# Performance work log

Hardware: AMD Instinct MI355X
Metric: run time of the kernel (lower is better)

Reference implementation:

```python
import jax, jax.numpy as jnp
import numpy as np

N_HEAD, DIM, D_K, D_V = 16, 1024, 64, 64
B, L = 4, 2048


def setup_inputs() -> dict:
    key = jax.random.key(0)
    ks = jax.random.split(key, 8)
    def xavier(k, shape, fan_in, fan_out):
        std = float(np.sqrt(2.0 / (fan_in + fan_out)))
        return jax.random.normal(k, shape, dtype=jnp.float32) * std
    return {
        "q": jax.random.normal(ks[0], (B, L, DIM), dtype=jnp.float32),
        "k": jax.random.normal(ks[1], (B, L, DIM), dtype=jnp.float32),
        "v": jax.random.normal(ks[2], (B, L, DIM), dtype=jnp.float32),
        "w_q": xavier(ks[3], (N_HEAD, DIM, D_K), DIM, D_K),
        "w_k": xavier(ks[4], (N_HEAD, DIM, D_K), DIM, D_K),
        "w_v": xavier(ks[5], (N_HEAD, DIM, D_V), DIM, D_V),
        "proj_w": xavier(ks[6], (DIM, N_HEAD * D_V), N_HEAD * D_V, DIM),
        "proj_b": jnp.zeros((DIM,), dtype=jnp.float32),
    }


def reference(q, k, v, w_q, w_k, w_v, proj_w, proj_b):
    batch, len_q, dim = q.shape
    # NOTE: original scales by sqrt(dim) (model dim), not sqrt(d_k)
    scale = jnp.asarray(np.sqrt(dim), dtype=q.dtype)
    # per-head projections: [h, b, q, dk]
    qh = jnp.einsum('bqd,hdk->hbqk', q, w_q)
    kh = jnp.einsum('bsd,hdk->hbsk', k, w_k)
    vh = jnp.einsum('bsd,hdv->hbsv', v, w_v)
    scores = jnp.einsum('hbqk,hbsk->hbqs', qh, kh) / scale
    attn = jax.nn.softmax(scores, axis=-1)
    out = jnp.einsum('hbqs,hbsv->hbqv', attn, vh)
    # concat heads along last dim: [b, q, h*dv] (head-major order, matching torch.cat(split))
    out = jnp.transpose(out, (1, 2, 0, 3)).reshape(batch, len_q, -1)
    # output projection (dropout is identity at eval)
    return out @ proj_w.T + proj_b
```

## Files before the change

kernel.cpp:

```cpp
#include <hip/hip_runtime.h>
#include <hip/hip_bf16.h>
#include <stdint.h>

#define NH 16
#define DM 1024
#define DKV 64
#define BB 4
#define LL 2048
#define MT (BB*LL)
#define NT (LL/64)

typedef __bf16 bf16;
typedef __bf16 bf16x8 __attribute__((ext_vector_type(8)));
typedef float f32x4 __attribute__((ext_vector_type(4)));
typedef float f32x16 __attribute__((ext_vector_type(16)));
typedef unsigned int u32x2 __attribute__((ext_vector_type(2)));
typedef unsigned int u32x4 __attribute__((ext_vector_type(4)));

__device__ __forceinline__ void gload_lds16(const void* g, void* l) {
  __builtin_amdgcn_global_load_lds(
      (const __attribute__((address_space(1))) unsigned int*)g,
      (__attribute__((address_space(3))) unsigned int*)l, 16, 0, 0);
}

__device__ __forceinline__ unsigned short bfbits(float x) {
  bf16 b = (bf16)x;
  return __builtin_bit_cast(unsigned short, b);
}

__device__ __forceinline__ float fast_exp2(float x) {
#if defined(__has_builtin)
#if __has_builtin(__builtin_amdgcn_exp2f)
  return __builtin_amdgcn_exp2f(x);
#else
  float r; asm("v_exp_f32 %0, %1" : "=v"(r) : "v"(x)); return r;
#endif
#else
  float r; asm("v_exp_f32 %0, %1" : "=v"(r) : "v"(x)); return r;
#endif
}

#if defined(__has_builtin)
#if __has_builtin(__builtin_amdgcn_permlane32_swap)
#define HAVE_PLSWAP 1
#endif
#endif

__device__ __forceinline__ u32x2 plswap(unsigned int a, unsigned int b, int hi) {
#ifdef HAVE_PLSWAP
  auto rr = __builtin_amdgcn_permlane32_swap(a, b, false, false);
  u32x2 r; r.x = rr[0]; r.y = rr[1];
  return r;
#else
  unsigned int pa = (unsigned int)__shfl_xor((int)a, 32);
  unsigned int pb_ = (unsigned int)__shfl_xor((int)b, 32);
  u32x2 r;
  r.x = hi ? pb_ : a;
  r.y = hi ? b : pa;
  return r;
#endif
}

__device__ __forceinline__ bf16x8 pack8(const f32x4& lo, const f32x4& hi2) {
  u32x4 u;
  u.x = (unsigned int)bfbits(lo[0]) | ((unsigned int)bfbits(lo[1]) << 16);
  u.y = (unsigned int)bfbits(lo[2]) | ((unsigned int)bfbits(lo[3]) << 16);
  u.z = (unsigned int)bfbits(hi2[0]) | ((unsigned int)bfbits(hi2[1]) << 16);
  u.w = (unsigned int)bfbits(hi2[2]) | ((unsigned int)bfbits(hi2[3]) << 16);
  return __builtin_bit_cast(bf16x8, u);
}

__global__ __launch_bounds__(256) void prep_w(const float* __restrict__ w0, const float* __restrict__ w1,
                                              const float* __restrict__ w2, const float* __restrict__ pw,
                                              bf16* __restrict__ o0, bf16* __restrict__ o1,
                                              bf16* __restrict__ o2, bf16* __restrict__ Wp) {
  __shared__ float t[64][65];
  if (blockIdx.z < 3) {
    const float* w = blockIdx.z == 0 ? w0 : (blockIdx.z == 1 ? w1 : w2);
    bf16* o = blockIdx.z == 0 ? o0 : (blockIdx.z == 1 ? o1 : o2);
    int h = blockIdx.y, d0 = blockIdx.x * 64;
    const float* src = w + ((size_t)h * DM + d0) * DKV;
    for (int i = threadIdx.x; i < 64 * 64; i += 256) {
      int r = i >> 6, c = i & 63;
      t[r][c] = src[(size_t)r * DKV + c];
    }
    __syncthreads();
    for (int i = threadIdx.x; i < 64 * 64; i += 256) {
      int kk = i >> 6, d = i & 63;
      o[((size_t)(h * 64 + kk)) * DM + d0 + d] = (bf16)t[d][kk];
    }
  } else {
    int base = ((blockIdx.y * 16 + blockIdx.x) * 256 + threadIdx.x) * 2;
#pragma unroll
    for (int e = 0; e < 2; ++e) {
      int i = base + e;
      const float4* p = (const float4*)pw + (size_t)i * 2;
      float4 a = p[0], b = p[1];
      bf16x8 r;
      r[0] = (bf16)a.x; r[1] = (bf16)a.y; r[2] = (bf16)a.z; r[3] = (bf16)a.w;
      r[4] = (bf16)b.x; r[5] = (bf16)b.y; r[6] = (bf16)b.z; r[7] = (bf16)b.w;
      *((bf16x8*)Wp + i) = r;
    }
  }
}

__global__ __launch_bounds__(256) void gemm_qkv(const float* __restrict__ Qf, const float* __restrict__ Kf,
                                                const float* __restrict__ Vf, const bf16* __restrict__ Wqt,
                                                const bf16* __restrict__ Wkt, const bf16* __restrict__ Wvt,
                                                bf16* __restrict__ QH, bf16* __restrict__ KH,
                                                bf16* __restrict__ VT) {
  __shared__ bf16 sA[128 * 64];
  __shared__ bf16 sB[128 * 64];
  const int bid = blockIdx.x;
  const int xcd = bid & 7;
  const int j   = bid >> 3;
  const int nb  = j & 7;
  const int t   = j >> 3;
  const int mb  = xcd + 8 * (t & 7);
  const int mode = t >> 3;
  const float* A = mode == 0 ? Qf : (mode == 1 ? Kf : Vf);
  const bf16* Bt = mode == 0 ? Wqt : (mode == 1 ? Wkt : Wvt);
  const int tid = threadIdx.x;
  const int w = tid >> 6, l = tid & 63;
  const int c = l & 15, g4 = l >> 4;
  const int wm = w >> 1, wn = w & 1;
  const int m0 = mb * 128, n0 = nb * 128;

  int grow[4], gsg[4];
#pragma unroll
  for (int jj = 0; jj < 4; ++jj) {
    int gi = jj * 256 + tid;
    grow[jj] = gi >> 3;
    gsg[jj] = (gi & 7) ^ (grow[jj] & 7);
  }

  f32x4 ra[4][2];
  u32x4 rbr[4];

  auto LOADA = [&](int kt) {
#pragma unroll
    for (int jj = 0; jj < 4; ++jj) {
      const float* s = A + (size_t)(m0 + grow[jj]) * 1024 + kt + gsg[jj] * 8;
      ra[jj][0] = *(const f32x4*)s;
      ra[jj][1] = *(const f32x4*)(s + 4);
    }
  };
  auto LOADB = [&](int kt) {
#pragma unroll
    for (int jj = 0; jj < 4; ++jj)
      rbr[jj] = *(const u32x4*)(Bt + (size_t)(n0 + grow[jj]) * 1024 + kt + gsg[jj] * 8);
  };
  auto WRITE = [&]() {
#pragma unroll
    for (int jj = 0; jj < 4; ++jj) {
      *(bf16x8*)((char*)sA + (jj * 256 + tid) * 16) = pack8(ra[jj][0], ra[jj][1]);
      *(u32x4*)((char*)sB + (jj * 256 + tid) * 16) = rbr[jj];
    }
  };

  f32x4 acc[4][4] = {};
  LOADA(0); LOADB(0);
  for (int it = 0; it < 16; ++it) {
    WRITE();
    if (it < 15) { LOADA((it + 1) * 64); LOADB((it + 1) * 64); }
    asm volatile("s_waitcnt lgkmcnt(0)" ::: "memory");
    __builtin_amdgcn_s_barrier();
#pragma unroll
    for (int ks = 0; ks < 2; ++ks) {
      bf16x8 af[4], bfr[4];
#pragma unroll
      for (int x = 0; x < 4; ++x) {
        int ar = wm * 64 + x * 16 + c;
        af[x] = *(const bf16x8*)((const char*)sA + ar * 128 + (((ks * 4 + g4) ^ (ar & 7)) * 16));
        int br = wn * 64 + x * 16 + c;
        bfr[x] = *(const bf16x8*)((const char*)sB + br * 128 + (((ks * 4 + g4) ^ (br & 7)) * 16));
      }
      __builtin_amdgcn_s_setprio(1);
#pragma unroll
      for (int x = 0; x < 4; ++x)
#pragma unroll
        for (int y = 0; y < 4; ++y)
          acc[x][y] = __builtin_amdgcn_mfma_f32_16x16x32_bf16(af[x], bfr[y], acc[x][y], 0, 0, 0);
      __builtin_amdgcn_s_setprio(0);
    }
    __builtin_amdgcn_s_barrier();
  }

  const int mm = m0 + wm * 64, nn = n0 + wn * 64;
  if (mode < 2) {
    bf16* O = mode == 0 ? QH : KH;
    const float s = (mode == 0) ? 0.03125f * 1.44269504088896f : 1.0f;
#pragma unroll
    for (int x = 0; x < 4; ++x)
#pragma unroll
      for (int y = 0; y < 4; ++y)
#pragma unroll
        for (int r = 0; r < 4; ++r) {
          int m = mm + x * 16 + g4 * 4 + r;
          int n = nn + y * 16 + c;
          O[(size_t)m * 1024 + n] = (bf16)(acc[x][y][r] * s);
        }
  } else {
    bf16* O = VT;
#pragma unroll
    for (int x = 0; x < 4; ++x)
#pragma unroll
      for (int y = 0; y < 4; ++y) {
        int mb2 = mm + x * 16 + g4 * 4;
        int n = nn + y * 16 + c;
        int bb2 = mb2 >> 11, sidx = mb2 & 2047;
        int hh2 = n >> 6, dv = n & 63;
        unsigned int u0 = bfbits(acc[x][y][0]) | ((unsigned int)bfbits(acc[x][y][1]) << 16);
        unsigned int u1 = bfbits(acc[x][y][2]) | ((unsigned int)bfbits(acc[x][y][3]) << 16);
        *(uint2*)(O + ((size_t)((hh2 * 4 + bb2) * 64 + dv)) * LL + sidx) = make_uint2(u0, u1);
      }
  }
}

__global__ __launch_bounds__(256) void gemm_proj(const bf16* __restrict__ A, const bf16* __restrict__ Bt,
                                                 float* __restrict__ Out, const float* __restrict__ bias) {
  __shared__ bf16 sA[128 * 64];
  __shared__ bf16 sB[128 * 64];
  const int bid = blockIdx.x;
  const int xcd = bid & 7;
  const int j = bid >> 3;
  const int nb = j & 7;
  const int mb = xcd + 8 * (j >> 3);
  const int tid = threadIdx.x;
  const int w = tid >> 6, l = tid & 63;
  const int c = l & 15, g4 = l >> 4;
  const int wm = w >> 1, wn = w & 1;
  const int m0 = mb * 128, n0 = nb * 128;

  f32x4 acc[4][4] = {};
  for (int kt = 0; kt < 1024; kt += 64) {
#pragma unroll
    for (int i = 0; i < 4; ++i) {
      int blk = i * 4 + w;
      int row = blk * 8 + (l >> 3);
      int g = (l & 7) ^ (row & 7);
      gload_lds16(A + ((size_t)(m0 + row)) * 1024 + kt + g * 8, (char*)sA + blk * 1024);
      gload_lds16(Bt + ((size_t)(n0 + row)) * 1024 + kt + g * 8, (char*)sB + blk * 1024);
    }
    __syncthreads();
#pragma unroll
    for (int ks = 0; ks < 2; ++ks) {
      bf16x8 af[4], bfr[4];
#pragma unroll
      for (int x = 0; x < 4; ++x) {
        int ar = wm * 64 + x * 16 + c;
        af[x] = *(const bf16x8*)((const char*)sA + ar * 128 + (((ks * 4 + g4) ^ (ar & 7)) * 16));
        int br = wn * 64 + x * 16 + c;
        bfr[x] = *(const bf16x8*)((const char*)sB + br * 128 + (((ks * 4 + g4) ^ (br & 7)) * 16));
      }
#pragma unroll
      for (int x = 0; x < 4; ++x)
#pragma unroll
        for (int y = 0; y < 4; ++y)
          acc[x][y] = __builtin_amdgcn_mfma_f32_16x16x32_bf16(af[x], bfr[y], acc[x][y], 0, 0, 0);
    }
    __syncthreads();
  }

  const int mm = m0 + wm * 64, nn = n0 + wn * 64;
#pragma unroll
  for (int x = 0; x < 4; ++x)
#pragma unroll
    for (int y = 0; y < 4; ++y)
#pragma unroll
      for (int r = 0; r < 4; ++r) {
        int m = mm + x * 16 + g4 * 4 + r;
        int n = nn + y * 16 + c;
        Out[(size_t)m * 1024 + n] = acc[x][y][r] + bias[n];
      }
}

__global__ __launch_bounds__(256, 2) void attn_kernel(const bf16* __restrict__ qh,
                                                      const bf16* __restrict__ kh,
                                                      const bf16* __restrict__ vt,
                                                      bf16* __restrict__ o) {
  __shared__ bf16 sK[4][64 * 64];
  __shared__ bf16 sV[4][64 * 64];
  const int tid = threadIdx.x, w = tid >> 6, l = tid & 63;
  const int c = l & 31, hi = l >> 5;
  const int bh = blockIdx.x, b = bh & 3, h = bh >> 2;
  const int q0 = blockIdx.y * 256 + w * 64;

  const bf16* qbase = qh + ((size_t)(b * LL)) * DM + h * 64;
  const bf16* kbase = kh + ((size_t)(b * LL)) * DM + h * 64;
  const bf16* vbase = vt + ((size_t)((h * 4 + b) * 64)) * LL;

  bf16x8 qfA[4], qfB[4];
#pragma unroll
  for (int ks = 0; ks < 4; ++ks) {
    qfA[ks] = *(const bf16x8*)(qbase + (size_t)(q0 + c) * DM + ks * 16 + hi * 8);
    qfB[ks] = *(const bf16x8*)(qbase + (size_t)(q0 + 32 + c) * DM + ks * 16 + hi * 8);
  }

  bf16x8 onesf;
#pragma unroll
  for (int i = 0; i < 8; ++i) onesf[i] = (bf16)1.0f;

  f32x16 oA0 = {}, oA1 = {}, oB0 = {}, oB1 = {};
  f32x16 lAa = {}, lBa = {};

  auto STAGE = [&](int bufi, int kv0) {
#pragma unroll
    for (int j = 0; j < 2; ++j) {
      int gi = w * 128 + j * 64 + l;
      int row = gi >> 3;
      int g = (gi & 7) ^ (row & 7);
      gload_lds16(kbase + (size_t)(kv0 + row) * DM + g * 8,
                  (char*)sK[bufi] + (w * 128 + j * 64) * 16);
      gload_lds16(vbase + (size_t)row * LL + kv0 + g * 8,
                  (char*)sV[bufi] + (w * 128 + j * 64) * 16);
    }
  };

  auto EXPPACK = [&](f32x16& st0, f32x16& st1, bf16x8* pb) {
#pragma unroll
    for (int r = 0; r < 16; ++r) st0[r] = fast_exp2(st0[r]);
#pragma unroll
    for (int r = 0; r < 16; ++r) st1[r] = fast_exp2(st1[r]);
#pragma unroll
    for (int t = 0; t < 2; ++t) {
      const f32x16& st = t ? st1 : st0;
      unsigned int u[4][2];
#pragma unroll
      for (int g2 = 0; g2 < 4; ++g2) {
        u[g2][0] = (unsigned int)bfbits(st[4 * g2 + 0]) | ((unsigned int)bfbits(st[4 * g2 + 1]) << 16);
        u[g2][1] = (unsigned int)bfbits(st[4 * g2 + 2]) | ((unsigned int)bfbits(st[4 * g2 + 3]) << 16);
      }
      u32x2 s0 = plswap(u[0][0], u[1][0], hi);
      u32x2 s1 = plswap(u[0][1], u[1][1], hi);
      u32x4 w0; w0.x = s0.x; w0.y = s1.x; w0.z = s0.y; w0.w = s1.y;
      pb[2 * t] = __builtin_bit_cast(bf16x8, w0);
      u32x2 s2 = plswap(u[2][0], u[3][0], hi);
      u32x2 s3 = plswap(u[2][1], u[3][1], hi);
      u32x4 w1; w1.x = s2.x; w1.y = s3.x; w1.z = s2.y; w1.w = s3.y;
      pb[2 * t + 1] = __builtin_bit_cast(bf16x8, w1);
    }
  };

  auto TILE = [&](int bufi) {
    const char* Kb = (const char*)sK[bufi];
    const char* Vb = (const char*)sV[bufi];

    bf16x8 kf[8];
#pragma unroll
    for (int ks = 0; ks < 4; ++ks) {
      int slot = ((ks * 2 + hi) ^ (c & 7)) * 16;
      kf[ks]     = *(const bf16x8*)(Kb + c * 128 + slot);
      kf[4 + ks] = *(const bf16x8*)(Kb + (32 + c) * 128 + slot);
    }
    f32x16 sA0 = {}, sA1 = {}, sB0 = {}, sB1 = {};
    __builtin_amdgcn_s_setprio(1);
#pragma unroll
    for (int ks = 0; ks < 4; ++ks) {
      sA0 = __builtin_amdgcn_mfma_f32_32x32x16_bf16(kf[ks],     qfA[ks], sA0, 0, 0, 0);
      sA1 = __builtin_amdgcn_mfma_f32_32x32x16_bf16(kf[4 + ks], qfA[ks], sA1, 0, 0, 0);
    }
#pragma unroll
    for (int ks = 0; ks < 4; ++ks) {
      sB0 = __builtin_amdgcn_mfma_f32_32x32x16_bf16(kf[ks],     qfB[ks], sB0, 0, 0, 0);
      sB1 = __builtin_amdgcn_mfma_f32_32x32x16_bf16(kf[4 + ks], qfB[ks], sB1, 0, 0, 0);
    }
    __builtin_amdgcn_s_setprio(0);

    bf16x8 pbA[4];
    EXPPACK(sA0, sA1, pbA);

    bf16x8 vf[8];
#pragma unroll
    for (int ks = 0; ks < 4; ++ks) {
      int slot = ((ks * 2 + hi) ^ (c & 7)) * 16;
      vf[ks]     = *(const bf16x8*)(Vb + c * 128 + slot);
      vf[4 + ks] = *(const bf16x8*)(Vb + (32 + c) * 128 + slot);
    }
    __builtin_amdgcn_s_setprio(1);
#pragma unroll
    for (int ks = 0; ks < 4; ++ks) {
      oA0 = __builtin_amdgcn_mfma_f32_32x32x16_bf16(vf[ks],     pbA[ks], oA0, 0, 0, 0);
      oA1 = __builtin_amdgcn_mfma_f32_32x32x16_bf16(vf[4 + ks], pbA[ks], oA1, 0, 0, 0);
      lAa = __builtin_amdgcn_mfma_f32_32x32x16_bf16(onesf,      pbA[ks], lAa, 0, 0, 0);
    }
    __builtin_amdgcn_s_setprio(0);

    bf16x8 pbB[4];
    EXPPACK(sB0, sB1, pbB);
    __builtin_amdgcn_s_setprio(1);
#pragma unroll
    for (int ks = 0; ks < 4; ++ks) {
      oB0 = __builtin_amdgcn_mfma_f32_32x32x16_bf16(vf[ks],     pbB[ks], oB0, 0, 0, 0);
      oB1 = __builtin_amdgcn_mfma_f32_32x32x16_bf16(vf[4 + ks], pbB[ks], oB1, 0, 0, 0);
      lBa = __builtin_amdgcn_mfma_f32_32x32x16_bf16(onesf,      pbB[ks], lBa, 0, 0, 0);
    }
    __builtin_amdgcn_s_setprio(0);
  };

  STAGE(0, 0);
  STAGE(1, 64);

  for (int wd = 0; wd < 16; ++wd) {
    __builtin_amdgcn_s_barrier();
    int t2 = 2 * wd + 2;
    if (t2 < NT) {
      STAGE(t2 & 3, t2 * 64);
      STAGE((t2 + 1) & 3, (t2 + 1) * 64);
      asm volatile("s_waitcnt vmcnt(8)" ::: "memory");
    } else {
      asm volatile("s_waitcnt vmcnt(0)" ::: "memory");
    }
    TILE((2 * wd) & 3);
    TILE((2 * wd + 1) & 3);
  }

  bf16* ob = o + ((size_t)(b * LL)) * DM + h * 64;
  {
    float inv = 1.0f / lAa[0];
#pragma unroll
    for (int dt = 0; dt < 2; ++dt) {
      const f32x16& oc = dt ? oA1 : oA0;
#pragma unroll
      for (int rg = 0; rg < 4; ++rg) {
        int dv0 = dt * 32 + rg * 8 + hi * 4;
        unsigned int u0 = (unsigned int)bfbits(oc[rg * 4 + 0] * inv) |
                          ((unsigned int)bfbits(oc[rg * 4 + 1] * inv) << 16);
        unsigned int u1 = (unsigned int)bfbits(oc[rg * 4 + 2] * inv) |
                          ((unsigned int)bfbits(oc[rg * 4 + 3] * inv) << 16);
        *(uint2*)(ob + (size_t)(q0 + c) * DM + dv0) = make_uint2(u0, u1);
      }
    }
  }
  {
    float inv = 1.0f / lBa[0];
#pragma unroll
    for (int dt = 0; dt < 2; ++dt) {
      const f32x16& oc = dt ? oB1 : oB0;
#pragma unroll
      for (int rg = 0; rg < 4; ++rg) {
        int dv0 = dt * 32 + rg * 8 + hi * 4;
        unsigned int u0 = (unsigned int)bfbits(oc[rg * 4 + 0] * inv) |
                          ((unsigned int)bfbits(oc[rg * 4 + 1] * inv) << 16);
        unsigned int u1 = (unsigned int)bfbits(oc[rg * 4 + 2] * inv) |
                          ((unsigned int)bfbits(oc[rg * 4 + 3] * inv) << 16);
        *(uint2*)(ob + (size_t)(q0 + 32 + c) * DM + dv0) = make_uint2(u0, u1);
      }
    }
  }
}

extern "C" void kernel_launch(void* const* d_in, const int* in_sizes, int n_in,
                              void* d_out, int out_size, void* d_ws, size_t ws_size,
                              hipStream_t stream) {
  const float* q  = (const float*)d_in[0];
  const float* k  = (const float*)d_in[1];
  const float* v  = (const float*)d_in[2];
  const float* wq = (const float*)d_in[3];
  const float* wk = (const float*)d_in[4];
  const float* wv = (const float*)d_in[5];
  const float* pw = (const float*)d_in[6];
  const float* pb = (const float*)d_in[7];
  float* out = (float*)d_out;

  char* ws = (char*)d_ws;
  const size_t SX = (size_t)MT * DM * 2;
  const size_t SW = (size_t)DM * DM * 2;
  bf16* Wqt = (bf16*)(ws);
  bf16* Wkt = (bf16*)(ws + SW);
  bf16* Wvt = (bf16*)(ws + 2 * SW);
  bf16* Wp  = (bf16*)(ws + 3 * SW);
  bf16* QH  = (bf16*)(ws + 4 * SW);
  bf16* KH  = (bf16*)(ws + 4 * SW + SX);
  bf16* VT  = (bf16*)(ws + 4 * SW + 2 * SX);
  bf16* OO  = (bf16*)(ws + 4 * SW + 3 * SX);

  prep_w<<<dim3(16, 16, 4), 256, 0, stream>>>(wq, wk, wv, pw, Wqt, Wkt, Wvt, Wp);

  gemm_qkv<<<dim3(1536), 256, 0, stream>>>(q, k, v, Wqt, Wkt, Wvt, QH, KH, VT);

  attn_kernel<<<dim3(64, 8), 256, 0, stream>>>(QH, KH, VT, OO);

  gemm_proj<<<dim3(512), 256, 0, stream>>>(OO, Wp, out, pb);
}
```

Before: 197.7 us.

## Stage QKV GEMM tiles via direct global-to-LDS loads with double buffering

Replaces the register-staged fp32 A loads (converted to bf16 before the LDS write) with global_load_lds DMA that writes raw fp32 A tiles and bf16 B tiles straight into double-buffered shared memory. The K step is halved to 32 so the fp32 tile fits, and the bf16 conversion moves to the LDS read side. The aim is to drop register staging and one barrier per iteration and overlap the next tile's load with the current MFMA work. The cost is twice as many loop iterations, more LDS read traffic for fp32 A, conversion work repeated by every wave that reads a tile, and a single barrier per iteration, which may not protect the buffer being refilled from waves still reading it.

```diff
diff --git a/kernel.cpp b/kernel.cpp
--- a/kernel.cpp
+++ b/kernel.cpp
@@ -109,8 +109,8 @@
                                                 const bf16* __restrict__ Wkt, const bf16* __restrict__ Wvt,
                                                 bf16* __restrict__ QH, bf16* __restrict__ KH,
                                                 bf16* __restrict__ VT) {
-  __shared__ bf16 sA[128 * 64];
-  __shared__ bf16 sB[128 * 64];
+  __shared__ float sA[2][128 * 32];
+  __shared__ bf16 sB[2][128 * 32];
   const int bid = blockIdx.x;
   const int xcd = bid & 7;
   const int j   = bid >> 3;
@@ -126,64 +126,55 @@
   const int wm = w >> 1, wn = w & 1;
   const int m0 = mb * 128, n0 = nb * 128;
 
-  int grow[4], gsg[4];
-#pragma unroll
-  for (int jj = 0; jj < 4; ++jj) {
-    int gi = jj * 256 + tid;
-    grow[jj] = gi >> 3;
-    gsg[jj] = (gi & 7) ^ (grow[jj] & 7);
-  }
-
-  f32x4 ra[4][2];
-  u32x4 rbr[4];
-
-  auto LOADA = [&](int kt) {
+  auto STAGE = [&](int bufi, int kt) {
 #pragma unroll
     for (int jj = 0; jj < 4; ++jj) {
-      const float* s = A + (size_t)(m0 + grow[jj]) * 1024 + kt + gsg[jj] * 8;
-      ra[jj][0] = *(const f32x4*)s;
-      ra[jj][1] = *(const f32x4*)(s + 4);
+      int gi = jj * 256 + tid;
+      int row = gi >> 3, slot = gi & 7;
+      gload_lds16(A + (size_t)(m0 + row) * 1024 + kt + (slot ^ (row & 7)) * 4,
+                  (char*)&sA[bufi][0] + (jj * 256 + w * 64) * 16);
+    }
+#pragma unroll
+    for (int jj = 0; jj < 2; ++jj) {
+      int gi = jj * 256 + tid;
+      int row = gi >> 2, slot = gi & 3;
+      gload_lds16(Bt + (size_t)(n0 + row) * 1024 + kt + (slot ^ (row & 3)) * 8,
+                  (char*)&sB[bufi][0] + (jj * 256 + w * 64) * 16);
     }
   };
-  auto LOADB = [&](int kt) {
-#pragma unroll
-    for (int jj = 0; jj < 4; ++jj)
-      rbr[jj] = *(const u32x4*)(Bt + (size_t)(n0 + grow[jj]) * 1024 + kt + gsg[jj] * 8);
-  };
-  auto WRITE = [&]() {
-#pragma unroll
-    for (int jj = 0; jj < 4; ++jj) {
-      *(bf16x8*)((char*)sA + (jj * 256 + tid) * 16) = pack8(ra[jj][0], ra[jj][1]);
-      *(u32x4*)((char*)sB + (jj * 256 + tid) * 16) = rbr[jj];
-    }
-  };
 
   f32x4 acc[4][4] = {};
-  LOADA(0); LOADB(0);
-  for (int it = 0; it < 16; ++it) {
-    WRITE();
-    if (it < 15) { LOADA((it + 1) * 64); LOADB((it + 1) * 64); }
-    asm volatile("s_waitcnt lgkmcnt(0)" ::: "memory");
+  STAGE(0, 0);
+  int buf = 0;
+  for (int it = 0; it < 32; ++it) {
     __builtin_amdgcn_s_barrier();
-#pragma unroll
-    for (int ks = 0; ks < 2; ++ks) {
-      bf16x8 af[4], bfr[4];
-#pragma unroll
-      for (int x = 0; x < 4; ++x) {
-        int ar = wm * 64 + x * 16 + c;
-        af[x] = *(const bf16x8*)((const char*)sA + ar * 128 + (((ks * 4 + g4) ^ (ar & 7)) * 16));
-        int br = wn * 64 + x * 16 + c;
-        bfr[x] = *(const bf16x8*)((const char*)sB + br * 128 + (((ks * 4 + g4) ^ (br & 7)) * 16));
-      }
-      __builtin_amdgcn_s_setprio(1);
-#pragma unroll
-      for (int x = 0; x < 4; ++x)
-#pragma unroll
-        for (int y = 0; y < 4; ++y)
-          acc[x][y] = __builtin_amdgcn_mfma_f32_16x16x32_bf16(af[x], bfr[y], acc[x][y], 0, 0, 0);
-      __builtin_amdgcn_s_setprio(0);
-    }
-    __builtin_amdgcn_s_barrier();
+    if (it + 1 < 32) {
+      STAGE(buf ^ 1, (it + 1) * 32);
+      asm volatile("s_waitcnt vmcnt(6)" ::: "memory");
+    } else {
+      asm volatile("s_waitcnt vmcnt(0)" ::: "memory");
+    }
+    const char* Ab = (const char*)&sA[buf][0];
+    const char* Bb = (const char*)&sB[buf][0];
+    bf16x8 af[4], bfr[4];
+#pragma unroll
+    for (int x = 0; x < 4; ++x) {
+      int ar = wm * 64 + x * 16 + c;
+      int p0 = g4 * 2;
+      f32x4 lo = *(const f32x4*)(Ab + ar * 128 + ((p0 ^ (ar & 7)) * 16));
+      f32x4 hi2 = *(const f32x4*)(Ab + ar * 128 + (((p0 + 1) ^ (ar & 7)) * 16));
+      af[x] = pack8(lo, hi2);
+      int br = wn * 64 + x * 16 + c;
+      bfr[x] = *(const bf16x8*)(Bb + br * 64 + ((g4 ^ (br & 3)) * 16));
+    }
+    __builtin_amdgcn_s_setprio(1);
+#pragma unroll
+    for (int x = 0; x < 4; ++x)
+#pragma unroll
+      for (int y = 0; y < 4; ++y)
+        acc[x][y] = __builtin_amdgcn_mfma_f32_16x16x32_bf16(af[x], bfr[y], acc[x][y], 0, 0, 0);
+    __builtin_amdgcn_s_setprio(0);
+    buf ^= 1;
   }
 
   const int mm = m0 + wm * 64, nn = n0 + wn * 64;
```

Result: slower. 212.3 us (+7.4%).
